# Performance work log

Hardware: AMD Instinct MI355X
Metric: run time of the kernel (lower is better)

The kernel has to match this reference:

```python
import jax, jax.numpy as jnp
import numpy as np

NUM_HEADS = 16
NEG_INF = jnp.float32(-1e9)


def setup_inputs() -> dict:
    key = jax.random.key(0)
    ks = jax.random.split(key, 4)
    B, N, C = 2, 2048, 1024
    s_in = 1.0 / np.sqrt(C)
    return {
        "x": jax.random.normal(ks[0], (B, N, C), jnp.float32),
        "attention_mask": jnp.ones((B, N, N), jnp.int32),
        "qkv_w": jax.random.normal(ks[1], (3 * C, C), jnp.float32) * s_in,
        "qkv_b": jnp.zeros((3 * C,), jnp.float32),
        "proj_w": jax.random.normal(ks[2], (C, C), jnp.float32) * s_in,
        "proj_b": jnp.zeros((C,), jnp.float32),
    }


def reference(x, attention_mask, qkv_w, qkv_b, proj_w, proj_b):
    B, N, C = x.shape
    H = NUM_HEADS
    D = C // H
    scale = D ** -0.5
    # fused QKV projection (torch Linear: x @ W^T + b)
    qkv = (x @ qkv_w.T + qkv_b).reshape(B, N, 3, H, D)
    qkv = jnp.transpose(qkv, (2, 0, 3, 1, 4))  # [3, B, H, N, D]
    q, k, v = qkv[0], qkv[1], qkv[2]
    # scaled dot-product scores [B, H, N, N]
    attn = jnp.einsum("bhnd,bhmd->bhnm", q, k) * scale
    # padding mask: [B, N, N] broadcast over heads
    attn = jnp.where(attention_mask[:, None, :, :] == 0, NEG_INF, attn)
    # causal mask
    causal = jnp.triu(jnp.ones((N, N), bool), k=1)
    attn = jnp.where(causal, NEG_INF, attn)
    w = jax.nn.softmax(attn, axis=-1)
    out = jnp.einsum("bhnm,bhmd->bhnd", w, v)
    out = jnp.transpose(out, (0, 2, 1, 3)).reshape(B, N, C)
    return out @ proj_w.T + proj_b
```

## Files before the change

### kernel.cpp

```cpp
#include <hip/hip_runtime.h>
#include <hip/hip_bf16.h>


typedef __bf16 bf16x8 __attribute__((ext_vector_type(8)));
typedef __bf16 bf16x4 __attribute__((ext_vector_type(4)));
typedef __bf16 bf16x2 __attribute__((ext_vector_type(2)));
typedef float  f32x4  __attribute__((ext_vector_type(4)));
typedef float  f32x16 __attribute__((ext_vector_type(16)));
typedef int    i32x4  __attribute__((ext_vector_type(4)));

#define MFMA16(a, b, c) __builtin_amdgcn_mfma_f32_16x16x32_bf16((a), (b), (c), 0, 0, 0)

__device__ __forceinline__ void async_copy16(const __bf16* g, __bf16* l) {
    __builtin_amdgcn_global_load_lds(
        (const __attribute__((address_space(1))) void*)g,
        (__attribute__((address_space(3))) void*)l,
        16, 0, 0);
}

__device__ __forceinline__ unsigned packbf(float a, float b) {
    union { bf16x2 v; unsigned u; } un;
    un.v[0] = (__bf16)a; un.v[1] = (__bf16)b;
    return un.u;
}

__global__ void f32_to_bf16_3k(const float* __restrict__ a, __bf16* __restrict__ ad, int na,
                               const float* __restrict__ b, __bf16* __restrict__ bd, int nb,
                               const float* __restrict__ c, __bf16* __restrict__ cd, int nc)
{
    int i = blockIdx.x * blockDim.x + threadIdx.x;
    const float* src; __bf16* dst; int j;
    if (i < na)            { src = a; dst = ad; j = i; }
    else if (i < na + nb)  { src = b; dst = bd; j = i - na; }
    else if (i < na + nb + nc) { src = c; dst = cd; j = i - na - nb; }
    else return;
    float4 v = reinterpret_cast<const float4*>(src)[j];
    bf16x4 o;
    o[0] = (__bf16)v.x; o[1] = (__bf16)v.y; o[2] = (__bf16)v.z; o[3] = (__bf16)v.w;
    reinterpret_cast<bf16x4*>(dst)[j] = o;
}

__global__ void mask_reduce_k(const int* __restrict__ mask, int* __restrict__ mflag) {
    __shared__ int ok;
    const int t = threadIdx.x;
    if (t == 0) ok = 1;
    __syncthreads();
    const int jt = blockIdx.x & 31;
    const int it = (blockIdx.x >> 5) & 31;
    const int b  = blockIdx.x >> 10;
    bool all1 = true;
#pragma unroll
    for (int c = 0; c < 4; ++c) {
        const int row = c * 16 + (t >> 4);
        const int col = (t & 15) * 4;
        const int4 v = *reinterpret_cast<const int4*>(
            &mask[((size_t)(b * 2048 + it * 64 + row)) * 2048 + jt * 64 + col]);
        all1 = all1 && v.x && v.y && v.z && v.w;
    }
    if (!all1) ok = 0;
    __syncthreads();
    if (t == 0) mflag[(b * 32 + it) * 32 + jt] = ok;
}

#define BAR() asm volatile("s_barrier" ::: "memory")
#define VM2() asm volatile("s_waitcnt vmcnt(2)" ::: "memory")
#define VM6() asm volatile("s_waitcnt vmcnt(6)" ::: "memory")

__global__ __launch_bounds__(512, 2) void gemm_qkv8_k(
    const __bf16* __restrict__ A, const __bf16* __restrict__ Bm,
    const float* __restrict__ bias,
    __bf16* __restrict__ qg, __bf16* __restrict__ kg, __bf16* __restrict__ vtg)
{
    __shared__ __align__(16) __bf16 As[2][16384];
    __shared__ __align__(16) __bf16 Bs[2][16384];

    const int t = threadIdx.x;
    const int lane = t & 63;
    const int w = t >> 6;
    const int wr = w >> 2, wc = w & 3;
    const int li = lane & 15, g = lane >> 4;

    const int bid = (blockIdx.x & 7) * 24 + (blockIdx.x >> 3);
    const int m0 = (bid / 12) << 8;
    const int n0 = (bid % 12) << 8;

    const int srow = t >> 3;
    const int scol = ((t & 7) ^ (srow & 7)) << 3;
    const __bf16* pA = A  + (size_t)(m0 + srow) * 1024 + scol;
    const __bf16* pB = Bm + (size_t)(n0 + srow) * 1024 + scol;
    __bf16* dA = &As[0][0] + t * 8;
    __bf16* dB = &Bs[0][0] + t * 8;

#define STAGE_A(BB, T, HH) do {                                                   \
    const size_t ro_ = (size_t)((HH) * 128) * 1024 + (size_t)(T) * 64;            \
    async_copy16(pA + ro_,         dA + (BB) * 16384 + (HH) * 8192);              \
    async_copy16(pA + ro_ + 65536, dA + (BB) * 16384 + (HH) * 8192 + 4096);       \
  } while (0)
#define STAGE_B(BB, T, HH) do {                                                   \
    const size_t ro_ = (size_t)((HH) * 128) * 1024 + (size_t)(T) * 64;            \
    async_copy16(pB + ro_,         dB + (BB) * 16384 + (HH) * 8192);              \
    async_copy16(pB + ro_ + 65536, dB + (BB) * 16384 + (HH) * 8192 + 4096);       \
  } while (0)

    const int aoff0 = ((0 + g) ^ (li & 7)) << 3;
    const int aoff1 = ((4 + g) ^ (li & 7)) << 3;
    const int abase = (wr * 128 + li) * 64;
    const int bbase = (wc * 64 + li) * 64;

    f32x4 acc[8][4] = {};
    bf16x8 a[4][2], b[2][2][2];

#define READ_A(BB, MH) do { _Pragma("unroll")                                     \
    for (int mi2 = 0; mi2 < 4; ++mi2) {                                           \
      const __bf16* p_ = &As[BB][abase + ((MH) * 4 + mi2) * 1024];                \
      a[mi2][0] = *reinterpret_cast<const bf16x8*>(p_ + aoff0);                   \
      a[mi2][1] = *reinterpret_cast<const bf16x8*>(p_ + aoff1); } } while (0)
#define READ_B(BB, NH) do { _Pragma("unroll")                                     \
    for (int ni2 = 0; ni2 < 2; ++ni2) {                                           \
      const __bf16* p_ = &Bs[BB][bbase + ((NH) * 2 + ni2) * 1024];                \
      b[NH][ni2][0] = *reinterpret_cast<const bf16x8*>(p_ + aoff0);               \
      b[NH][ni2][1] = *reinterpret_cast<const bf16x8*>(p_ + aoff1); } } while (0)
#define MFMA_QUAD(MH, NH) do {                                                    \
    __builtin_amdgcn_s_setprio(1);                                                \
    _Pragma("unroll") for (int mi2 = 0; mi2 < 4; ++mi2)                           \
    _Pragma("unroll") for (int ni2 = 0; ni2 < 2; ++ni2) {                         \
      f32x4 c_ = acc[(MH) * 4 + mi2][(NH) * 2 + ni2];                             \
      c_ = MFMA16(a[mi2][0], b[NH][ni2][0], c_);                                  \
      c_ = MFMA16(a[mi2][1], b[NH][ni2][1], c_);                                  \
      acc[(MH) * 4 + mi2][(NH) * 2 + ni2] = c_; }                                 \
    __builtin_amdgcn_s_setprio(0); } while (0)

#define KTILE(BB, T) do {                                                         \
    const int Tn_  = ((T) + 1 < 16) ? (T) + 1 : 15;                               \
    const int Tn2_ = ((T) + 2 < 16) ? (T) + 2 : 15;                               \
    STAGE_A((BB) ^ 1, Tn_, 1);                                                    \
    READ_A(BB, 0); READ_B(BB, 0);                                                 \
    BAR(); MFMA_QUAD(0, 0); BAR();                                                \
    STAGE_B((BB) ^ 1, Tn_, 0);                                                    \
    READ_B(BB, 1);                                                                \
    BAR(); MFMA_QUAD(0, 1); BAR();                                                \
    STAGE_B((BB) ^ 1, Tn_, 1);                                                    \
    READ_A(BB, 1);                                                                \
    BAR(); MFMA_QUAD(1, 0); BAR();                                                \
    STAGE_A((BB), Tn2_, 0);                                                       \
    VM2(); BAR(); MFMA_QUAD(1, 1); BAR();                                         \
  } while (0)

    STAGE_A(0, 0, 0); STAGE_A(0, 0, 1);
    STAGE_B(0, 0, 0); STAGE_B(0, 0, 1);
    STAGE_A(1, 1, 0);
    VM2(); BAR();

#pragma unroll 1
    for (int jj = 0; jj < 8; ++jj) {
        KTILE(0, 2 * jj);
        KTILE(1, 2 * jj + 1);
    }

    const int nbase = n0 + wc * 64;
    const int s = nbase >> 10;
    const int headg = (m0 >> 11) * 16 + ((nbase & 1023) >> 6);
    const int mrow = (m0 & 2047) + wr * 128 + g * 4;
    float bv[4];
#pragma unroll
    for (int ni = 0; ni < 4; ++ni) bv[ni] = bias[nbase + ni * 16 + li];

    if (s == 2) {
#pragma unroll
        for (int mi = 0; mi < 8; ++mi) {
#pragma unroll
            for (int ni = 0; ni < 4; ++ni) {
                bf16x4 st;
#pragma unroll
                for (int r = 0; r < 4; ++r) st[r] = (__bf16)(acc[mi][ni][r] + bv[ni]);
                *reinterpret_cast<bf16x4*>(
                    &vtg[((size_t)(headg * 64) + ni * 16 + li) * 2048 + mrow + mi * 16]) = st;
            }
        }
    } else {
        __bf16* og = (s == 0) ? qg : kg;
        const float sc = (s == 0) ? 0.18033688f : 1.0f;
#pragma unroll
        for (int mi = 0; mi < 8; ++mi) {
#pragma unroll
            for (int r = 0; r < 4; ++r) {
                __bf16* rp = og + ((size_t)headg * 2048 + mrow + mi * 16 + r) * 64;
#pragma unroll
                for (int ni = 0; ni < 4; ++ni)
                    rp[ni * 16 + li] = (__bf16)((acc[mi][ni][r] + bv[ni]) * sc);
            }
        }
    }
#undef KTILE
#undef MFMA_QUAD
#undef READ_A
#undef READ_B
#undef STAGE_A
#undef STAGE_B
}

__global__ __launch_bounds__(256) void gemm_proj_k(
    const __bf16* __restrict__ A, const __bf16* __restrict__ Bm,
    const float* __restrict__ bias, float* __restrict__ outf)
{
    __shared__ __align__(16) __bf16 As[3][8192];
    __shared__ __align__(16) __bf16 Bs[3][4096];
    const int t = threadIdx.x;
    const int lane = t & 63, w = t >> 6;
    const int li = lane & 15, g = lane >> 4;
    const int wr = w >> 1, wc = w & 1;
    const int sw7 = li & 7;
    const int bid = (blockIdx.x & 7) * 64 + (blockIdx.x >> 3);
    const int m0 = (bid >> 4) << 7;
    const int n0 = (bid & 15) << 6;

#define PSTAGE(BUF, KT) do {                                                      \
    _Pragma("unroll")                                                             \
    for (int c_ = 0; c_ < 4; ++c_) {                                              \
        const int row_ = c_ * 32 + (t >> 3);                                      \
        async_copy16(A + (size_t)(m0 + row_) * 1024 + ((KT) << 6)                 \
                       + (((t & 7) ^ (row_ & 7)) << 3),                           \
                     &As[BUF][0] + c_ * 2048 + t * 8);                            \
    }                                                                             \
    _Pragma("unroll")                                                             \
    for (int c_ = 0; c_ < 2; ++c_) {                                              \
        const int row_ = c_ * 32 + (t >> 3);                                      \
        async_copy16(Bm + (size_t)(n0 + row_) * 1024 + ((KT) << 6)                \
                       + (((t & 7) ^ (row_ & 7)) << 3),                           \
                     &Bs[BUF][0] + c_ * 2048 + t * 8);                            \
    }                                                                             \
} while (0)

    f32x4 acc[4][2] = {};

    PSTAGE(0, 0);
    int cur = 0;
    for (int kt = 0; kt < 16; ++kt) {
        int nxt = cur + 1; if (nxt == 3) nxt = 0;
        if (kt < 15) {
            PSTAGE(nxt, kt + 1);
            VM6();
        } else {
            asm volatile("s_waitcnt vmcnt(0)" ::: "memory");
        }
        __builtin_amdgcn_sched_barrier(0);
        __builtin_amdgcn_s_barrier();
        __builtin_amdgcn_sched_barrier(0);

        bf16x8 af[4][2], bf[2][2];
#pragma unroll
        for (int mi = 0; mi < 4; ++mi) {
            const int ra = wr * 64 + mi * 16 + li;
#pragma unroll
            for (int kk = 0; kk < 2; ++kk)
                af[mi][kk] = *reinterpret_cast<const bf16x8*>(
                    (char*)&As[cur][0] + ra * 128 + (((kk * 4 + g) ^ sw7) << 4));
        }
#pragma unroll
        for (int ni = 0; ni < 2; ++ni) {
            const int rb = wc * 32 + ni * 16 + li;
#pragma unroll
            for (int kk = 0; kk < 2; ++kk)
                bf[ni][kk] = *reinterpret_cast<const bf16x8*>(
                    (char*)&Bs[cur][0] + rb * 128 + (((kk * 4 + g) ^ sw7) << 4));
        }
        __builtin_amdgcn_s_setprio(1);
#pragma unroll
        for (int mi = 0; mi < 4; ++mi)
#pragma unroll
            for (int ni = 0; ni < 2; ++ni) {
                f32x4 c_ = acc[mi][ni];
                c_ = MFMA16(af[mi][0], bf[ni][0], c_);
                c_ = MFMA16(af[mi][1], bf[ni][1], c_);
                acc[mi][ni] = c_;
            }
        __builtin_amdgcn_s_setprio(0);
        cur = nxt;
    }
#undef PSTAGE

#pragma unroll
    for (int mi = 0; mi < 4; ++mi) {
#pragma unroll
        for (int ni = 0; ni < 2; ++ni) {
            const int n = n0 + wc * 32 + ni * 16 + li;
            const float bv = bias[n];
#pragma unroll
            for (int r = 0; r < 4; ++r) {
                const int m = m0 + wr * 64 + mi * 16 + g * 4 + r;
                outf[(size_t)m * 1024 + n] = acc[mi][ni][r] + bv;
            }
        }
    }
}

__global__ __launch_bounds__(512) void attn_k(
    const __bf16* __restrict__ qg, const __bf16* __restrict__ kg,
    const __bf16* __restrict__ vtg, const int* __restrict__ mflag,
    const int* __restrict__ mask, __bf16* __restrict__ ao)
{
    __shared__ __align__(16) __bf16 Ks[4][4096];
    __shared__ __align__(16) __bf16 Vs[4][4096];
    __shared__ __align__(16) __bf16 Ps[8][1024];
    const int t = threadIdx.x;
    const int w = t >> 6, lane = t & 63;
    const int li = lane & 15, g = lane >> 4;
    const int xcd = blockIdx.x & 7;
    const int idx = blockIdx.x >> 3;
    const int hg  = xcd * 4 + (idx & 3);
    const int q_  = idx >> 2;
    const int band = (q_ < 8) ? (15 - q_) : (q_ - 8);
    const int bI = hg >> 4, hI = hg & 15;
    const int iq = band * 128 + w * 16 + li;
    const int mydiag = 2 * band + (w >> 2);
    const int ktmax = 2 * band + 1;
    const int rowt = 2 * band + (w >> 2);
    const size_t hoff = (size_t)hg * (2048 * 64);
    const __bf16* qh = qg + hoff;
    const __bf16* kh = kg + hoff;
    const __bf16* vh = vtg + hoff;
    char* pw = (char*)&Ps[w][0];
    const int sw7 = li & 7;

    bf16x8 qf[2];
#pragma unroll
    for (int half = 0; half < 2; ++half)
        qf[half] = *reinterpret_cast<const bf16x8*>(&qh[(size_t)iq * 64 + half * 32 + g * 8]);

    f32x4 o[4] = {};
    float mrun = -1e30f, lrun = 0.0f;

#define STAGE(BUF, KT) do {                                                       \
    const int p_ = t * 16;                                                        \
    const int row_ = p_ >> 7, sl_ = (p_ >> 4) & 7;                                \
    const int gc_ = (sl_ ^ (row_ & 7)) << 3;                                      \
    async_copy16(kh + (size_t)(((KT) << 6) + row_) * 64 + gc_,                    \
                 (__bf16*)((char*)(&Ks[0][0]) + (BUF) * 8192 + p_));              \
    async_copy16(vh + (size_t)row_ * 2048 + ((KT) << 6) + gc_,                    \
                 (__bf16*)((char*)(&Vs[0][0]) + (BUF) * 8192 + p_));              \
} while (0)

    STAGE(0, 0);
    STAGE(1, 1);
    VM2();
    __builtin_amdgcn_s_barrier();

    int cur = 0;
    for (int kt = 0; kt <= ktmax; ++kt) {
        if (kt + 2 <= ktmax) {
            STAGE((cur + 2) & 3, kt + 2);
            VM2();
        } else {
            asm volatile("s_waitcnt vmcnt(0)" ::: "memory");
        }
        __builtin_amdgcn_sched_barrier(0);
        __builtin_amdgcn_s_barrier();
        __builtin_amdgcn_sched_barrier(0);
        if (kt <= mydiag) {
            const char* kb = (char*)&Ks[0][0] + cur * 8192;
            const char* vb = (char*)&Vs[0][0] + cur * 8192;
            f32x4 s[4] = {};
            __builtin_amdgcn_s_setprio(1);
#pragma unroll
            for (int kb_ = 0; kb_ < 4; ++kb_) {
                const int row = kb_ * 16 + li;
#pragma unroll
                for (int half = 0; half < 2; ++half) {
                    bf16x8 kf = *reinterpret_cast<const bf16x8*>(
                        kb + row * 128 + (((half * 4 + g) ^ sw7) << 4));
                    s[kb_] = MFMA16(kf, qf[half], s[kb_]);
                }
            }
            __builtin_amdgcn_s_setprio(0);
            const bool pflag = (mflag[(bI * 32 + rowt) * 32 + kt] == 0);
            if (pflag || kt == mydiag) {
                const int jb = kt * 64;
#pragma unroll
                for (int kb_ = 0; kb_ < 4; ++kb_)
#pragma unroll
                    for (int r = 0; r < 4; ++r) {
                        const int j0 = jb + kb_ * 16 + 4 * g + r;
                        float v0 = s[kb_][r];
                        if (j0 > iq ||
                            (pflag && mask[((size_t)(bI * 2048 + iq)) * 2048 + j0] == 0))
                            v0 = -1e30f;
                        s[kb_][r] = v0;
                    }
            }
            float mt = fmaxf(fmaxf(s[0][0], s[0][1]), fmaxf(s[0][2], s[0][3]));
#pragma unroll
            for (int kb_ = 1; kb_ < 4; ++kb_)
                mt = fmaxf(mt, fmaxf(fmaxf(s[kb_][0], s[kb_][1]),
                                     fmaxf(s[kb_][2], s[kb_][3])));
            mt = fmaxf(mt, __shfl_xor(mt, 16));
            mt = fmaxf(mt, __shfl_xor(mt, 32));
            if (!__all(mt <= mrun + 8.0f)) {
                const float mn = fmaxf(mrun, mt);
                const float alpha = exp2f(mrun - mn);
#pragma unroll
                for (int df = 0; df < 4; ++df)
#pragma unroll
                    for (int r = 0; r < 4; ++r) o[df][r] *= alpha;
                lrun *= alpha;
                mrun = mn;
            }
#pragma unroll
            for (int kb_ = 0; kb_ < 4; ++kb_)
#pragma unroll
                for (int r = 0; r < 4; ++r) {
                    const float p = exp2f(s[kb_][r] - mrun);
                    s[kb_][r] = p;
                    lrun += p;
                }
#pragma unroll
            for (int kb_ = 0; kb_ < 4; ++kb_) {
                const unsigned lo = packbf(s[kb_][0], s[kb_][1]);
                const unsigned hi = packbf(s[kb_][2], s[kb_][3]);
                *reinterpret_cast<uint2*>(
                    pw + li * 128 + (((2 * kb_ + (g >> 1)) ^ sw7) << 4) + ((g & 1) << 3)) =
                    make_uint2(lo, hi);
            }
            bf16x8 pb[2];
#pragma unroll
            for (int ks = 0; ks < 2; ++ks)
                pb[ks] = *reinterpret_cast<const bf16x8*>(
                    pw + li * 128 + (((4 * ks + g) ^ sw7) << 4));
            __builtin_amdgcn_s_setprio(1);
#pragma unroll
            for (int df = 0; df < 4; ++df) {
                const int vrow = df * 16 + li;
#pragma unroll
                for (int ks = 0; ks < 2; ++ks) {
                    bf16x8 vf = *reinterpret_cast<const bf16x8*>(
                        vb + vrow * 128 + (((4 * ks + g) ^ sw7) << 4));
                    o[df] = MFMA16(vf, pb[ks], o[df]);
                }
            }
            __builtin_amdgcn_s_setprio(0);
        }
        cur = (cur + 1) & 3;
    }
#undef STAGE

    lrun += __shfl_xor(lrun, 16);
    lrun += __shfl_xor(lrun, 32);
    const float inv = 1.0f / lrun;
    __bf16* aor = ao + ((size_t)(bI * 2048 + iq)) * 1024 + hI * 64 + g * 4;
#pragma unroll
    for (int df = 0; df < 4; ++df) {
        bf16x4 st;
#pragma unroll
        for (int r = 0; r < 4; ++r) st[r] = (__bf16)(o[df][r] * inv);
        *reinterpret_cast<bf16x4*>(&aor[df * 16]) = st;
    }
}

extern "C" void kernel_launch(void* const* d_in, const int* in_sizes, int n_in,
                              void* d_out, int out_size, void* d_ws, size_t ws_size,
                              hipStream_t stream)
{
    const float* x      = (const float*)d_in[0];
    const int*   mask   = (const int*)d_in[1];
    const float* qkv_w  = (const float*)d_in[2];
    const float* qkv_b  = (const float*)d_in[3];
    const float* proj_w = (const float*)d_in[4];
    const float* proj_b = (const float*)d_in[5];
    float* out = (float*)d_out;

    char* ws = (char*)d_ws;
    __bf16* xb    = (__bf16*)(ws + 0);
    __bf16* wqkv  = (__bf16*)(ws + 8388608);
    __bf16* wproj = (__bf16*)(ws + 14680064);
    __bf16* qg    = (__bf16*)(ws + 16777216);
    __bf16* kg    = (__bf16*)(ws + 25165824);
    __bf16* vtg   = (__bf16*)(ws + 33554432);
    __bf16* ao    = (__bf16*)(ws + 41943040);
    int*    mflag = (int*)(ws + 50331648);

    f32_to_bf16_3k<<<8192, 256, 0, stream>>>(x, xb, 1048576,
                                             qkv_w, wqkv, 786432,
                                             proj_w, wproj, 262144);
    mask_reduce_k<<<2 * 32 * 32, 256, 0, stream>>>(mask, mflag);
    gemm_qkv8_k<<<192, 512, 0, stream>>>(xb, wqkv, qkv_b, qg, kg, vtg);
    attn_k<<<512, 512, 0, stream>>>(qg, kg, vtg, mflag, mask, ao);
    gemm_proj_k<<<512, 256, 0, stream>>>(ao, wproj, proj_b, out);
}
```

Baseline: 121.4 us.

## Switch attention to 32x32 MFMA with 4 waves and register-shuffled P

The attention kernel now uses 32x32x16 bf16 MFMAs with each wave owning 32 query rows, so blocks shrink from 8 to 4 waves. The P matrix is moved from the LDS round-trip into MFMA operand layout with cross-half lane shuffles, and the per-wave Ps shared buffer is removed. Each thread stages two K/V chunks per tile and the wait counts change to match. The aim is fewer MFMA issues and no LDS traffic for P, at the cost of larger accumulators, more register pressure and fewer waves per block to hide latency.

```diff
diff --git a/kernel.cpp b/kernel.cpp
--- a/kernel.cpp
+++ b/kernel.cpp
@@ -10,6 +10,7 @@
 typedef int    i32x4  __attribute__((ext_vector_type(4)));
 
 #define MFMA16(a, b, c) __builtin_amdgcn_mfma_f32_16x16x32_bf16((a), (b), (c), 0, 0, 0)
+#define MFMA32(a, b, c) __builtin_amdgcn_mfma_f32_32x32x16_bf16((a), (b), (c), 0, 0, 0)
 
 __device__ __forceinline__ void async_copy16(const __bf16* g, __bf16* l) {
     __builtin_amdgcn_global_load_lds(
@@ -64,6 +65,7 @@
 
 #define BAR() asm volatile("s_barrier" ::: "memory")
 #define VM2() asm volatile("s_waitcnt vmcnt(2)" ::: "memory")
+#define VM4() asm volatile("s_waitcnt vmcnt(4)" ::: "memory")
 #define VM6() asm volatile("s_waitcnt vmcnt(6)" ::: "memory")
 
 __global__ __launch_bounds__(512, 2) void gemm_qkv8_k(
@@ -294,62 +296,63 @@
     }
 }
 
-__global__ __launch_bounds__(512) void attn_k(
+__global__ __launch_bounds__(256) void attn_k(
     const __bf16* __restrict__ qg, const __bf16* __restrict__ kg,
     const __bf16* __restrict__ vtg, const int* __restrict__ mflag,
     const int* __restrict__ mask, __bf16* __restrict__ ao)
 {
     __shared__ __align__(16) __bf16 Ks[4][4096];
     __shared__ __align__(16) __bf16 Vs[4][4096];
-    __shared__ __align__(16) __bf16 Ps[8][1024];
     const int t = threadIdx.x;
     const int w = t >> 6, lane = t & 63;
-    const int li = lane & 15, g = lane >> 4;
+    const int h = lane >> 5, l31 = lane & 31;
     const int xcd = blockIdx.x & 7;
     const int idx = blockIdx.x >> 3;
     const int hg  = xcd * 4 + (idx & 3);
     const int q_  = idx >> 2;
     const int band = (q_ < 8) ? (15 - q_) : (q_ - 8);
     const int bI = hg >> 4, hI = hg & 15;
-    const int iq = band * 128 + w * 16 + li;
-    const int mydiag = 2 * band + (w >> 2);
+    const int q0w = band * 128 + w * 32;
+    const int iq = q0w + l31;
+    const int mydiag = 2 * band + (w >> 1);
     const int ktmax = 2 * band + 1;
-    const int rowt = 2 * band + (w >> 2);
     const size_t hoff = (size_t)hg * (2048 * 64);
     const __bf16* qh = qg + hoff;
     const __bf16* kh = kg + hoff;
     const __bf16* vh = vtg + hoff;
-    char* pw = (char*)&Ps[w][0];
-    const int sw7 = li & 7;
-
-    bf16x8 qf[2];
-#pragma unroll
-    for (int half = 0; half < 2; ++half)
-        qf[half] = *reinterpret_cast<const bf16x8*>(&qh[(size_t)iq * 64 + half * 32 + g * 8]);
-
-    f32x4 o[4] = {};
+    const int rsw = l31 & 7;
+
+    bf16x8 qf[4];
+#pragma unroll
+    for (int ds2 = 0; ds2 < 4; ++ds2)
+        qf[ds2] = *reinterpret_cast<const bf16x8*>(&qh[(size_t)iq * 64 + ds2 * 16 + h * 8]);
+
+    f32x16 o0 = {}, o1 = {};
     float mrun = -1e30f, lrun = 0.0f;
 
 #define STAGE(BUF, KT) do {                                                       \
-    const int p_ = t * 16;                                                        \
-    const int row_ = p_ >> 7, sl_ = (p_ >> 4) & 7;                                \
-    const int gc_ = (sl_ ^ (row_ & 7)) << 3;                                      \
-    async_copy16(kh + (size_t)(((KT) << 6) + row_) * 64 + gc_,                    \
-                 (__bf16*)((char*)(&Ks[0][0]) + (BUF) * 8192 + p_));              \
-    async_copy16(vh + (size_t)row_ * 2048 + ((KT) << 6) + gc_,                    \
-                 (__bf16*)((char*)(&Vs[0][0]) + (BUF) * 8192 + p_));              \
+    _Pragma("unroll")                                                             \
+    for (int c_ = 0; c_ < 2; ++c_) {                                              \
+        const int p_ = c_ * 4096 + t * 16;                                        \
+        const int prow_ = p_ >> 7;                                                \
+        const int pslot_ = ((p_ >> 4) & 7) ^ (prow_ & 7);                         \
+        async_copy16(kh + (size_t)(((KT) << 6) + prow_) * 64 + (pslot_ << 3),     \
+                     (__bf16*)((char*)(&Ks[0][0]) + (BUF) * 8192 + p_));          \
+        async_copy16(vh + (size_t)prow_ * 2048 + ((KT) << 6) + (pslot_ << 3),     \
+                     (__bf16*)((char*)(&Vs[0][0]) + (BUF) * 8192 + p_));          \
+    }                                                                             \
 } while (0)
 
     STAGE(0, 0);
     STAGE(1, 1);
-    VM2();
+    VM4();
     __builtin_amdgcn_s_barrier();
 
     int cur = 0;
     for (int kt = 0; kt <= ktmax; ++kt) {
         if (kt + 2 <= ktmax) {
             STAGE((cur + 2) & 3, kt + 2);
-            VM2();
+            VM4();
         } else {
             asm volatile("s_waitcnt vmcnt(0)" ::: "memory");
         }
@@ -359,82 +362,84 @@
         if (kt <= mydiag) {
             const char* kb = (char*)&Ks[0][0] + cur * 8192;
             const char* vb = (char*)&Vs[0][0] + cur * 8192;
-            f32x4 s[4] = {};
+            f32x16 s0 = {}, s1 = {};
             __builtin_amdgcn_s_setprio(1);
 #pragma unroll
-            for (int kb_ = 0; kb_ < 4; ++kb_) {
-                const int row = kb_ * 16 + li;
-#pragma unroll
-                for (int half = 0; half < 2; ++half) {
-                    bf16x8 kf = *reinterpret_cast<const bf16x8*>(
-                        kb + row * 128 + (((half * 4 + g) ^ sw7) << 4));
-                    s[kb_] = MFMA16(kf, qf[half], s[kb_]);
-                }
+            for (int ds2 = 0; ds2 < 4; ++ds2) {
+                const int sl = ds2 * 2 + h;
+                bf16x8 kf0 = *reinterpret_cast<const bf16x8*>(
+                    kb + l31 * 128 + (((sl ^ rsw)) << 4));
+                bf16x8 kf1 = *reinterpret_cast<const bf16x8*>(
+                    kb + (32 + l31) * 128 + (((sl ^ rsw)) << 4));
+                s0 = MFMA32(kf0, qf[ds2], s0);
+                s1 = MFMA32(kf1, qf[ds2], s1);
             }
             __builtin_amdgcn_s_setprio(0);
-            const bool pflag = (mflag[(bI * 32 + rowt) * 32 + kt] == 0);
+            const bool pflag = (mflag[(bI * 32 + mydiag) * 32 + kt] == 0);
             if (pflag || kt == mydiag) {
                 const int jb = kt * 64;
 #pragma unroll
-                for (int kb_ = 0; kb_ < 4; ++kb_)
-#pragma unroll
-                    for (int r = 0; r < 4; ++r) {
-                        const int j0 = jb + kb_ * 16 + 4 * g + r;
-                        float v0 = s[kb_][r];
-                        if (j0 > iq ||
-                            (pflag && mask[((size_t)(bI * 2048 + iq)) * 2048 + j0] == 0))
-                            v0 = -1e30f;
-                        s[kb_][r] = v0;
-                    }
-            }
-            float mt = fmaxf(fmaxf(s[0][0], s[0][1]), fmaxf(s[0][2], s[0][3]));
-#pragma unroll
-            for (int kb_ = 1; kb_ < 4; ++kb_)
-                mt = fmaxf(mt, fmaxf(fmaxf(s[kb_][0], s[kb_][1]),
-                                     fmaxf(s[kb_][2], s[kb_][3])));
-            mt = fmaxf(mt, __shfl_xor(mt, 16));
+                for (int r = 0; r < 16; ++r) {
+                    const int cr = (r & 3) + 8 * (r >> 2) + 4 * h;
+                    const int j0 = jb + cr, j1 = jb + 32 + cr;
+                    float v0 = s0[r], v1 = s1[r];
+                    if (j0 > iq || (pflag && mask[((size_t)(bI * 2048 + iq)) * 2048 + j0] == 0)) v0 = -1e30f;
+                    if (j1 > iq || (pflag && mask[((size_t)(bI * 2048 + iq)) * 2048 + j1] == 0)) v1 = -1e30f;
+                    s0[r] = v0; s1[r] = v1;
+                }
+            }
+            float mt = s0[0];
+#pragma unroll
+            for (int r = 1; r < 16; ++r) mt = fmaxf(mt, s0[r]);
+#pragma unroll
+            for (int r = 0; r < 16; ++r) mt = fmaxf(mt, s1[r]);
             mt = fmaxf(mt, __shfl_xor(mt, 32));
             if (!__all(mt <= mrun + 8.0f)) {
                 const float mn = fmaxf(mrun, mt);
                 const float alpha = exp2f(mrun - mn);
 #pragma unroll
-                for (int df = 0; df < 4; ++df)
-#pragma unroll
-                    for (int r = 0; r < 4; ++r) o[df][r] *= alpha;
+                for (int r = 0; r < 16; ++r) { o0[r] *= alpha; o1[r] *= alpha; }
                 lrun *= alpha;
                 mrun = mn;
             }
 #pragma unroll
-            for (int kb_ = 0; kb_ < 4; ++kb_)
-#pragma unroll
-                for (int r = 0; r < 4; ++r) {
-                    const float p = exp2f(s[kb_][r] - mrun);
-                    s[kb_][r] = p;
-                    lrun += p;
+            for (int r = 0; r < 16; ++r) {
+                const float p0 = exp2f(s0[r] - mrun); s0[r] = p0; lrun += p0;
+                const float p1 = exp2f(s1[r] - mrun); s1[r] = p1; lrun += p1;
+            }
+            bf16x8 pa[4];
+#pragma unroll
+            for (int ks = 0; ks < 4; ++ks) {
+                const int c0 = (ks & 1) * 8;
+                unsigned A0, A1, B0, B1;
+                if (ks < 2) {
+                    A0 = packbf(s0[c0 + 0], s0[c0 + 1]); A1 = packbf(s0[c0 + 2], s0[c0 + 3]);
+                    B0 = packbf(s0[c0 + 4], s0[c0 + 5]); B1 = packbf(s0[c0 + 6], s0[c0 + 7]);
+                } else {
+                    A0 = packbf(s1[c0 + 0], s1[c0 + 1]); A1 = packbf(s1[c0 + 2], s1[c0 + 3]);
+                    B0 = packbf(s1[c0 + 4], s1[c0 + 5]); B1 = packbf(s1[c0 + 6], s1[c0 + 7]);
                 }
-#pragma unroll
-            for (int kb_ = 0; kb_ < 4; ++kb_) {
-                const unsigned lo = packbf(s[kb_][0], s[kb_][1]);
-                const unsigned hi = packbf(s[kb_][2], s[kb_][3]);
-                *reinterpret_cast<uint2*>(
-                    pw + li * 128 + (((2 * kb_ + (g >> 1)) ^ sw7) << 4) + ((g & 1) << 3)) =
-                    make_uint2(lo, hi);
-            }
-            bf16x8 pb[2];
-#pragma unroll
-            for (int ks = 0; ks < 2; ++ks)
-                pb[ks] = *reinterpret_cast<const bf16x8*>(
-                    pw + li * 128 + (((4 * ks + g) ^ sw7) << 4));
+                const unsigned Z0 = h ? A0 : B0;
+                const unsigned Z1 = h ? A1 : B1;
+                const unsigned X0 = (unsigned)__shfl_xor((int)Z0, 32);
+                const unsigned X1 = (unsigned)__shfl_xor((int)Z1, 32);
+                i32x4 wv;
+                wv[0] = (int)(h ? X0 : A0);
+                wv[1] = (int)(h ? X1 : A1);
+                wv[2] = (int)(h ? B0 : X0);
+                wv[3] = (int)(h ? B1 : X1);
+                pa[ks] = __builtin_bit_cast(bf16x8, wv);
+            }
             __builtin_amdgcn_s_setprio(1);
 #pragma unroll
-            for (int df = 0; df < 4; ++df) {
-                const int vrow = df * 16 + li;
-#pragma unroll
-                for (int ks = 0; ks < 2; ++ks) {
-                    bf16x8 vf = *reinterpret_cast<const bf16x8*>(
-                        vb + vrow * 128 + (((4 * ks + g) ^ sw7) << 4));
-                    o[df] = MFMA16(vf, pb[ks], o[df]);
-                }
+            for (int ks = 0; ks < 4; ++ks) {
+                const int sl = ks * 2 + h;
+                bf16x8 vf0 = *reinterpret_cast<const bf16x8*>(
+                    vb + l31 * 128 + (((sl ^ rsw)) << 4));
+                bf16x8 vf1 = *reinterpret_cast<const bf16x8*>(
+                    vb + (32 + l31) * 128 + (((sl ^ rsw)) << 4));
+                o0 = MFMA32(vf0, pa[ks], o0);
+                o1 = MFMA32(vf1, pa[ks], o1);
             }
             __builtin_amdgcn_s_setprio(0);
         }
@@ -442,16 +447,19 @@
     }
 #undef STAGE
 
-    lrun += __shfl_xor(lrun, 16);
     lrun += __shfl_xor(lrun, 32);
     const float inv = 1.0f / lrun;
-    __bf16* aor = ao + ((size_t)(bI * 2048 + iq)) * 1024 + hI * 64 + g * 4;
-#pragma unroll
-    for (int df = 0; df < 4; ++df) {
-        bf16x4 st;
-#pragma unroll
-        for (int r = 0; r < 4; ++r) st[r] = (__bf16)(o[df][r] * inv);
-        *reinterpret_cast<bf16x4*>(&aor[df * 16]) = st;
+    __bf16* aor = ao + ((size_t)(bI * 2048 + iq)) * 1024 + hI * 64 + h * 4;
+#pragma unroll
+    for (int rq = 0; rq < 4; ++rq) {
+        bf16x4 st0, st1;
+#pragma unroll
+        for (int c2 = 0; c2 < 4; ++c2) {
+            st0[c2] = (__bf16)(o0[rq * 4 + c2] * inv);
+            st1[c2] = (__bf16)(o1[rq * 4 + c2] * inv);
+        }
+        *reinterpret_cast<bf16x4*>(&aor[rq * 8])      = st0;
+        *reinterpret_cast<bf16x4*>(&aor[32 + rq * 8]) = st1;
     }
 }
 
@@ -482,6 +490,6 @@
                                              proj_w, wproj, 262144);
     mask_reduce_k<<<2 * 32 * 32, 256, 0, stream>>>(mask, mflag);
     gemm_qkv8_k<<<192, 512, 0, stream>>>(xb, wqkv, qkv_b, qg, kg, vtg);
-    attn_k<<<512, 512, 0, stream>>>(qg, kg, vtg, mflag, mask, ao);
+    attn_k<<<512, 256, 0, stream>>>(qg, kg, vtg, mflag, mask, ao);
     gemm_proj_k<<<512, 256, 0, stream>>>(ao, wproj, proj_b, out);
 }
```

Result: slower. 139.8 us (+15.2%).
